# Kernel tuning notes

Hardware: AMD Instinct MI355X
Metric: run time of the kernel (lower is better)

Reference implementation:

```python
import jax, jax.numpy as jnp
import numpy as np

N_NODES = 100000


def _add_self_loops(edge_index, n):
    loops = jnp.arange(n, dtype=edge_index.dtype)
    src = jnp.concatenate([edge_index[0], loops])
    dst = jnp.concatenate([edge_index[1], loops])
    return src, dst


def _gcn_norm(src, dst, n):
    # symmetric normalization with unit edge weights (edge_weight=None)
    w = jnp.ones(src.shape[0], dtype=jnp.float32)
    deg = jax.ops.segment_sum(w, dst, num_segments=n)  # in-degree at dst (col)
    dinv = jnp.where(deg > 0, jax.lax.rsqrt(jnp.maximum(deg, 1.0)), 0.0)
    return dinv[src] * w * dinv[dst]


def _gcn_conv(x, W, b, src, dst, norm, n):
    h = x @ W                              # [N, F_out] linear first (as in PyG GCNConv)
    msg = h[src] * norm[:, None]           # gather + per-edge scale
    agg = jax.ops.segment_sum(msg, dst, num_segments=n)  # scatter-add at dst
    return agg + b


def setup_inputs() -> dict:
    key = jax.random.key(0)
    k1, k2, k3, k4 = jax.random.split(key, 4)
    x = jax.random.normal(k1, (N_NODES, 128), dtype=jnp.float32)
    edge_index = jax.random.randint(k2, (2, 1600000), 0, N_NODES, dtype=jnp.int64)
    W1 = jax.random.normal(k3, (128, 64), dtype=jnp.float32) * 0.08
    b1 = jnp.zeros((64,), dtype=jnp.float32)
    W2 = jax.random.normal(k4, (64, 40), dtype=jnp.float32) * 0.1
    b2 = jnp.zeros((40,), dtype=jnp.float32)
    return {"x": x, "edge_index": edge_index, "W1": W1, "b1": b1, "W2": W2, "b2": b2}


def reference(x, edge_index, W1, b1, W2, b2):
    n = x.shape[0]
    src, dst = _add_self_loops(edge_index, n)
    norm = _gcn_norm(src, dst, n)
    h = _gcn_conv(x, W1, b1, src, dst, norm, n)
    h = jax.nn.relu(h)
    # dropout is identity in eval mode (training=False)
    out = _gcn_conv(h, W2, b2, src, dst, norm, n)
    return out
```

## Files before the change

### kernel.cpp

```cpp
#include <hip/hip_runtime.h>
#include <hip/hip_fp16.h>


#define NPB   128
#define NBCAP 1024


__global__ void k_zero(int* __restrict__ p, int m) {
    int i = blockIdx.x * blockDim.x + threadIdx.x;
    if (i < m) p[i] = 0;
}

__global__ __launch_bounds__(256) void k_hist(const int* __restrict__ dst, int E,
                                              int* __restrict__ bcnt, int nb) {
    __shared__ int h[NBCAP];
    for (int i = threadIdx.x; i < nb; i += 256) h[i] = 0;
    __syncthreads();
    int stride = gridDim.x * 256;
    for (int e = blockIdx.x * 256 + threadIdx.x; e < E; e += stride)
        atomicAdd(&h[dst[e] >> 7], 1);
    __syncthreads();
    for (int i = threadIdx.x; i < nb; i += 256)
        if (h[i]) atomicAdd(&bcnt[i], h[i]);
}

__global__ __launch_bounds__(1024) void k_scan_nb(const int* __restrict__ bcnt,
                                                  int* __restrict__ bbase,
                                                  int* __restrict__ bcur, int nb) {
    __shared__ int tmp[NBCAP];
    int t = threadIdx.x;
    int v = (t < nb) ? bcnt[t] : 0;
    tmp[t] = v;
    __syncthreads();
    for (int ofs = 1; ofs < NBCAP; ofs <<= 1) {
        int u = (t >= ofs) ? tmp[t - ofs] : 0;
        __syncthreads();
        if (t >= ofs) tmp[t] += u;
        __syncthreads();
    }
    if (t < nb) {
        int ex = tmp[t] - v;
        bbase[t] = ex;
        bcur[t] = ex;
        if (t == nb - 1) bbase[nb] = tmp[t];
    }
}

__global__ __launch_bounds__(256) void k_binpass(const int* __restrict__ src,
                                                 const int* __restrict__ dst,
                                                 int* __restrict__ bcur,
                                                 int* __restrict__ pairs,
                                                 int nb, int E) {
    __shared__ int lh[NBCAP];
    __shared__ int lbase[NBCAP];
    for (int i = threadIdx.x; i < nb; i += 256) lh[i] = 0;
    __syncthreads();
    int base = blockIdx.x * 4096;
    int pk[16], bb[16];
#pragma unroll
    for (int k = 0; k < 16; ++k) {
        int e = base + k * 256 + threadIdx.x;
        if (e < E) {
            int d = dst[e];
            int b = d >> 7;
            bb[k] = b;
            pk[k] = src[e] | ((d & (NPB - 1)) << 17);
            atomicAdd(&lh[b], 1);
        } else bb[k] = -1;
    }
    __syncthreads();
    for (int i = threadIdx.x; i < nb; i += 256) {
        int c = lh[i];
        lbase[i] = c ? atomicAdd(&bcur[i], c) : 0;
        lh[i] = 0;
    }
    __syncthreads();
#pragma unroll
    for (int k = 0; k < 16; ++k) {
        if (bb[k] >= 0) {
            int r = atomicAdd(&lh[bb[k]], 1);
            pairs[lbase[bb[k]] + r] = pk[k];
        }
    }
}

__global__ __launch_bounds__(256) void k_bucket_build(const int* __restrict__ pairs,
                                                      const int* __restrict__ bbase,
                                                      int* __restrict__ off,
                                                      int* __restrict__ csrc,
                                                      float* __restrict__ dinv,
                                                      int n, int nb) {
    __shared__ int deg[NPB], sc[NPB], cur[NPB];
    int t = threadIdx.x;
    int bid = blockIdx.x;
    int node0 = bid * NPB;
    int ebeg = bbase[bid], eend = bbase[bid + 1];
    if (t < NPB) deg[t] = 0;
    __syncthreads();
    for (int e = ebeg + t; e < eend; e += 256)
        atomicAdd(&deg[pairs[e] >> 17], 1);
    __syncthreads();
    if (t < NPB) sc[t] = deg[t];
    __syncthreads();
    for (int ofs = 1; ofs < NPB; ofs <<= 1) {
        int u = (t < NPB && t >= ofs) ? sc[t - ofs] : 0;
        __syncthreads();
        if (t < NPB && t >= ofs) sc[t] += u;
        __syncthreads();
    }
    if (t < NPB) {
        int ex = sc[t] - deg[t];
        cur[t] = ex;
        int node = node0 + t;
        if (node < n) {
            off[node] = ebeg + ex;
            dinv[node] = rsqrtf((float)(deg[t] + 1));
        }
    }
    if (t == 0 && bid == nb - 1) off[n] = eend;
    __syncthreads();
    for (int e = ebeg + t; e < eend; e += 256) {
        int pkv = pairs[e];
        int r = atomicAdd(&cur[pkv >> 17], 1);
        csrc[ebeg + r] = pkv & 0x1FFFF;
    }
}


union pk2 { __half2 h[2]; uint2 u; };
union pk4 { __half2 h[4]; uint4 u; };

#define F4ADD(a, b) { (a).x += (b).x; (a).y += (b).y; (a).z += (b).z; (a).w += (b).w; }

__device__ __forceinline__ void acc8f(float4& lo, float4& hi, uint4 u) {
    __half2 h0 = *(__half2*)&u.x, h1 = *(__half2*)&u.y;
    __half2 h2v = *(__half2*)&u.z, h3v = *(__half2*)&u.w;
    float2 f0 = __half22float2(h0), f1 = __half22float2(h1);
    float2 f2 = __half22float2(h2v), f3 = __half22float2(h3v);
    lo.x += f0.x; lo.y += f0.y; lo.z += f1.x; lo.w += f1.y;
    hi.x += f2.x; hi.y += f2.y; hi.z += f3.x; hi.w += f3.y;
}

__device__ __forceinline__ void redstep(float4& lo, float4& hi, int delta, bool act) {
    float4 rl, rh;
    rl.x = __shfl_down(lo.x, delta); rl.y = __shfl_down(lo.y, delta);
    rl.z = __shfl_down(lo.z, delta); rl.w = __shfl_down(lo.w, delta);
    rh.x = __shfl_down(hi.x, delta); rh.y = __shfl_down(hi.y, delta);
    rh.z = __shfl_down(hi.z, delta); rh.w = __shfl_down(hi.w, delta);
    if (act) { F4ADD(lo, rl); F4ADD(hi, rh); }
}


__global__ __launch_bounds__(256) void k_gemm1_h(const float* __restrict__ x,
                                                 const float* __restrict__ W,
                                                 __half* __restrict__ h, int n,
                                                 const float* __restrict__ dinv) {
    __shared__ float Ws[128 * 64];
    __shared__ float xsT[128 * 64];
    const int tid = threadIdx.x;
    const int row0 = blockIdx.x * 64;
    {
        const float4* Wg = (const float4*)W;
        float4* Wl = (float4*)Ws;
#pragma unroll
        for (int t = 0; t < 8; ++t) Wl[tid + t * 256] = Wg[tid + t * 256];
    }
    {
        int r = tid & 63, g = tid >> 6;
        int row = row0 + r;
        const float4* xr = (const float4*)(x + (size_t)row * 128);
#pragma unroll
        for (int t = 0; t < 8; ++t) {
            int k0 = g * 32 + t * 4;
            float4 v = (row < n) ? xr[k0 >> 2] : make_float4(0.f, 0.f, 0.f, 0.f);
            xsT[(k0 + 0) * 64 + r] = v.x;
            xsT[(k0 + 1) * 64 + r] = v.y;
            xsT[(k0 + 2) * 64 + r] = v.z;
            xsT[(k0 + 3) * 64 + r] = v.w;
        }
    }
    __syncthreads();

    const int tc = tid & 15;
    const int rg = tid >> 4;
    float acc[4][4];
#pragma unroll
    for (int i = 0; i < 4; ++i)
#pragma unroll
        for (int j = 0; j < 4; ++j) acc[i][j] = 0.f;

#pragma unroll 4
    for (int k = 0; k < 128; ++k) {
        float4 a = *(const float4*)&xsT[k * 64 + rg * 4];
        float4 b = *(const float4*)&Ws[k * 64 + tc * 4];
        acc[0][0] += a.x * b.x; acc[0][1] += a.x * b.y; acc[0][2] += a.x * b.z; acc[0][3] += a.x * b.w;
        acc[1][0] += a.y * b.x; acc[1][1] += a.y * b.y; acc[1][2] += a.y * b.z; acc[1][3] += a.y * b.w;
        acc[2][0] += a.z * b.x; acc[2][1] += a.z * b.y; acc[2][2] += a.z * b.z; acc[2][3] += a.z * b.w;
        acc[3][0] += a.w * b.x; acc[3][1] += a.w * b.y; acc[3][2] += a.w * b.z; acc[3][3] += a.w * b.w;
    }

#pragma unroll
    for (int i = 0; i < 4; ++i) {
        int row = row0 + rg * 4 + i;
        if (row < n) {
            float dd = dinv[row];
            pk2 p;
            p.h[0] = __floats2half2_rn(acc[i][0] * dd, acc[i][1] * dd);
            p.h[1] = __floats2half2_rn(acc[i][2] * dd, acc[i][3] * dd);
            *(uint2*)&h[(size_t)row * 64 + tc * 4] = p.u;
        }
    }
}

__global__ __launch_bounds__(256) void k_gemm2_h(const __half* __restrict__ agg,
                                                 const float* __restrict__ W2,
                                                 __half* __restrict__ h2, int n,
                                                 const float* __restrict__ dinv) {
    __shared__ float Ws[64 * 40];
    __shared__ float hsT[64 * 64];
    const int tid = threadIdx.x;
    const int row0 = blockIdx.x * 64;
    {
        const float4* Wg = (const float4*)W2;
        float4* Wl = (float4*)Ws;
        for (int i = tid; i < 640; i += 256) Wl[i] = Wg[i];
    }
    {
        int r = tid & 63, g = tid >> 6;
        int row = row0 + r;
        const __half* ar = agg + (size_t)row * 64;
#pragma unroll
        for (int t = 0; t < 4; ++t) {
            int k0 = g * 16 + t * 4;
            float4 v = make_float4(0.f, 0.f, 0.f, 0.f);
            if (row < n) {
                uint2 u = *(const uint2*)(ar + k0);
                __half2 h0 = *(__half2*)&u.x, h1 = *(__half2*)&u.y;
                float2 f0 = __half22float2(h0), f1 = __half22float2(h1);
                v = make_float4(f0.x, f0.y, f1.x, f1.y);
            }
            hsT[(k0 + 0) * 64 + r] = v.x > 0.f ? v.x : 0.f;
            hsT[(k0 + 1) * 64 + r] = v.y > 0.f ? v.y : 0.f;
            hsT[(k0 + 2) * 64 + r] = v.z > 0.f ? v.z : 0.f;
            hsT[(k0 + 3) * 64 + r] = v.w > 0.f ? v.w : 0.f;
        }
    }
    __syncthreads();

    const int tc = tid & 15;
    const int rg = tid >> 4;
    if (tc < 10) {
        float acc[4][4];
#pragma unroll
        for (int i = 0; i < 4; ++i)
#pragma unroll
            for (int j = 0; j < 4; ++j) acc[i][j] = 0.f;

#pragma unroll 4
        for (int k = 0; k < 64; ++k) {
            float4 a = *(const float4*)&hsT[k * 64 + rg * 4];
            float4 b = *(const float4*)&Ws[k * 40 + tc * 4];
            acc[0][0] += a.x * b.x; acc[0][1] += a.x * b.y; acc[0][2] += a.x * b.z; acc[0][3] += a.x * b.w;
            acc[1][0] += a.y * b.x; acc[1][1] += a.y * b.y; acc[1][2] += a.y * b.z; acc[1][3] += a.y * b.w;
            acc[2][0] += a.z * b.x; acc[2][1] += a.z * b.y; acc[2][2] += a.z * b.z; acc[2][3] += a.z * b.w;
            acc[3][0] += a.w * b.x; acc[3][1] += a.w * b.y; acc[3][2] += a.w * b.z; acc[3][3] += a.w * b.w;
        }

#pragma unroll
        for (int i = 0; i < 4; ++i) {
            int row = row0 + rg * 4 + i;
            if (row < n) {
                float dd = dinv[row];
                pk2 p;
                p.h[0] = __floats2half2_rn(acc[i][0] * dd, acc[i][1] * dd);
                p.h[1] = __floats2half2_rn(acc[i][2] * dd, acc[i][3] * dd);
                *(uint2*)&h2[(size_t)row * 40 + tc * 4] = p.u;
            }
        }
    }
}


__global__ __launch_bounds__(256) void k_gather1_h(const __half* __restrict__ hs,
                                                   const int* __restrict__ off,
                                                   const int* __restrict__ csrc,
                                                   const float* __restrict__ dinv,
                                                   const float* __restrict__ bias1,
                                                   __half* __restrict__ agg1,
                                                   int n, int nwaves) {
    int wid = (blockIdx.x * 256 + threadIdx.x) >> 6;
    int lane = threadIdx.x & 63;
    int g = lane >> 3, q = lane & 7;
    for (int node = wid; node < n; node += nwaves) {
        int beg = off[node], end = off[node + 1];
        float4 a0 = make_float4(0.f, 0.f, 0.f, 0.f);
        float4 a1 = make_float4(0.f, 0.f, 0.f, 0.f);
        float4 c0 = make_float4(0.f, 0.f, 0.f, 0.f);
        float4 c1 = make_float4(0.f, 0.f, 0.f, 0.f);
        int j = beg;
        for (; j + 16 <= end; j += 16) {
            int s0 = csrc[j + g];
            int s1 = csrc[j + 8 + g];
            uint4 u0 = *(const uint4*)(hs + ((size_t)s0 << 6) + (q << 3));
            uint4 u1 = *(const uint4*)(hs + ((size_t)s1 << 6) + (q << 3));
            acc8f(a0, a1, u0);
            acc8f(c0, c1, u1);
        }
        for (; j + 8 <= end; j += 8) {
            int s0 = csrc[j + g];
            uint4 u0 = *(const uint4*)(hs + ((size_t)s0 << 6) + (q << 3));
            acc8f(a0, a1, u0);
        }
        if (j + g < end) {
            int s0 = csrc[j + g];
            uint4 u0 = *(const uint4*)(hs + ((size_t)s0 << 6) + (q << 3));
            acc8f(a0, a1, u0);
        }
        F4ADD(a0, c0); F4ADD(a1, c1);
        redstep(a0, a1, 32, lane < 32);
        redstep(a0, a1, 16, lane < 16);
        redstep(a0, a1, 8,  lane < 8);
        if (lane < 8) {
            float dd = dinv[node];
            uint4 us = *(const uint4*)(hs + ((size_t)node << 6) + (q << 3));
            float4 slo = make_float4(0.f, 0.f, 0.f, 0.f);
            float4 shi = make_float4(0.f, 0.f, 0.f, 0.f);
            acc8f(slo, shi, us);
            float4 blo = *(const float4*)(bias1 + q * 8);
            float4 bhi = *(const float4*)(bias1 + q * 8 + 4);
            pk4 p;
            p.h[0] = __floats2half2_rn((a0.x + slo.x) * dd + blo.x,
                                       (a0.y + slo.y) * dd + blo.y);
            p.h[1] = __floats2half2_rn((a0.z + slo.z) * dd + blo.z,
                                       (a0.w + slo.w) * dd + blo.w);
            p.h[2] = __floats2half2_rn((a1.x + shi.x) * dd + bhi.x,
                                       (a1.y + shi.y) * dd + bhi.y);
            p.h[3] = __floats2half2_rn((a1.z + shi.z) * dd + bhi.z,
                                       (a1.w + shi.w) * dd + bhi.w);
            *(uint4*)&agg1[((size_t)node << 6) + (q << 3)] = p.u;
        }
    }
}

__global__ __launch_bounds__(256) void k_gather2_h(const __half* __restrict__ h2s,
                                                   const int* __restrict__ off,
                                                   const int* __restrict__ csrc,
                                                   const float* __restrict__ dinv,
                                                   const float* __restrict__ b2,
                                                   float* __restrict__ out,
                                                   int n, int nwaves) {
    int wid = (blockIdx.x * 256 + threadIdx.x) >> 6;
    int lane = threadIdx.x & 63;
    int g = lane / 5;
    int q = lane - g * 5;
    bool act = lane < 60;
    for (int node = wid; node < n; node += nwaves) {
        int beg = off[node], end = off[node + 1];
        float4 a0 = make_float4(0.f, 0.f, 0.f, 0.f);
        float4 a1 = make_float4(0.f, 0.f, 0.f, 0.f);
        int j = beg;
        for (; j + 12 <= end; j += 12) {
            if (act) {
                int s0 = csrc[j + g];
                uint4 u0 = *(const uint4*)(h2s + (size_t)s0 * 40 + q * 8);
                acc8f(a0, a1, u0);
            }
        }
        if (act && j + g < end) {
            int s0 = csrc[j + g];
            uint4 u0 = *(const uint4*)(h2s + (size_t)s0 * 40 + q * 8);
            acc8f(a0, a1, u0);
        }
        redstep(a0, a1, 30, lane < 30);
        redstep(a0, a1, 15, lane < 15);
        redstep(a0, a1, 10, lane < 5);
        redstep(a0, a1, 5,  lane < 5);
        if (lane < 5) {
            float dd = dinv[node];
            uint4 us = *(const uint4*)(h2s + (size_t)node * 40 + lane * 8);
            float4 slo = make_float4(0.f, 0.f, 0.f, 0.f);
            float4 shi = make_float4(0.f, 0.f, 0.f, 0.f);
            acc8f(slo, shi, us);
            float4 blo = *(const float4*)(b2 + lane * 8);
            float4 bhi = *(const float4*)(b2 + lane * 8 + 4);
            float4 o0, o1;
            o0.x = (a0.x + slo.x) * dd + blo.x;
            o0.y = (a0.y + slo.y) * dd + blo.y;
            o0.z = (a0.z + slo.z) * dd + blo.z;
            o0.w = (a0.w + slo.w) * dd + blo.w;
            o1.x = (a1.x + shi.x) * dd + bhi.x;
            o1.y = (a1.y + shi.y) * dd + bhi.y;
            o1.z = (a1.z + shi.z) * dd + bhi.z;
            o1.w = (a1.w + shi.w) * dd + bhi.w;
            *(float4*)&out[(size_t)node * 40 + lane * 8] = o0;
            *(float4*)&out[(size_t)node * 40 + lane * 8 + 4] = o1;
        }
    }
}


__global__ void k_init_deg(float* __restrict__ deg, int n) {
    int i = blockIdx.x * blockDim.x + threadIdx.x;
    if (i < n) deg[i] = 1.0f;
}

__global__ void k_deg(const int* __restrict__ dst, int E, float* __restrict__ deg) {
    int i = blockIdx.x * blockDim.x + threadIdx.x;
    if (i < E) atomicAdd(&deg[dst[i]], 1.0f);
}

__global__ void k_rsqrt(float* __restrict__ deg, int n) {
    int i = blockIdx.x * blockDim.x + threadIdx.x;
    if (i < n) deg[i] = rsqrtf(deg[i]);
}

__global__ __launch_bounds__(256) void k_gemm1_f(const float* __restrict__ x,
                                                 const float* __restrict__ W,
                                                 float* __restrict__ h, int n) {
    __shared__ float Ws[128 * 64];
    __shared__ float xsT[128 * 64];
    const int tid = threadIdx.x;
    const int row0 = blockIdx.x * 64;
    {
        const float4* Wg = (const float4*)W;
        float4* Wl = (float4*)Ws;
#pragma unroll
        for (int t = 0; t < 8; ++t) Wl[tid + t * 256] = Wg[tid + t * 256];
    }
    {
        int r = tid & 63, g = tid >> 6;
        int row = row0 + r;
        const float4* xr = (const float4*)(x + (size_t)row * 128);
#pragma unroll
        for (int t = 0; t < 8; ++t) {
            int k0 = g * 32 + t * 4;
            float4 v = (row < n) ? xr[k0 >> 2] : make_float4(0.f, 0.f, 0.f, 0.f);
            xsT[(k0 + 0) * 64 + r] = v.x;
            xsT[(k0 + 1) * 64 + r] = v.y;
            xsT[(k0 + 2) * 64 + r] = v.z;
            xsT[(k0 + 3) * 64 + r] = v.w;
        }
    }
    __syncthreads();
    const int tc = tid & 15;
    const int rg = tid >> 4;
    float acc[4][4];
#pragma unroll
    for (int i = 0; i < 4; ++i)
#pragma unroll
        for (int j = 0; j < 4; ++j) acc[i][j] = 0.f;
#pragma unroll 4
    for (int k = 0; k < 128; ++k) {
        float4 a = *(const float4*)&xsT[k * 64 + rg * 4];
        float4 b = *(const float4*)&Ws[k * 64 + tc * 4];
        acc[0][0] += a.x * b.x; acc[0][1] += a.x * b.y; acc[0][2] += a.x * b.z; acc[0][3] += a.x * b.w;
        acc[1][0] += a.y * b.x; acc[1][1] += a.y * b.y; acc[1][2] += a.y * b.z; acc[1][3] += a.y * b.w;
        acc[2][0] += a.z * b.x; acc[2][1] += a.z * b.y; acc[2][2] += a.z * b.z; acc[2][3] += a.z * b.w;
        acc[3][0] += a.w * b.x; acc[3][1] += a.w * b.y; acc[3][2] += a.w * b.z; acc[3][3] += a.w * b.w;
    }
#pragma unroll
    for (int i = 0; i < 4; ++i) {
        int row = row0 + rg * 4 + i;
        if (row < n)
            *(float4*)&h[(size_t)row * 64 + tc * 4] =
                make_float4(acc[i][0], acc[i][1], acc[i][2], acc[i][3]);
    }
}

__global__ __launch_bounds__(256) void k_gemm2_f(const float* __restrict__ agg,
                                                 const float* __restrict__ W2,
                                                 float* __restrict__ h2, int n) {
    __shared__ float Ws[64 * 40];
    __shared__ float hsT[64 * 64];
    const int tid = threadIdx.x;
    const int row0 = blockIdx.x * 64;
    {
        const float4* Wg = (const float4*)W2;
        float4* Wl = (float4*)Ws;
        for (int i = tid; i < 640; i += 256) Wl[i] = Wg[i];
    }
    {
        int r = tid & 63, g = tid >> 6;
        int row = row0 + r;
        const float4* ar = (const float4*)(agg + (size_t)row * 64);
#pragma unroll
        for (int t = 0; t < 4; ++t) {
            int k0 = g * 16 + t * 4;
            float4 v = (row < n) ? ar[k0 >> 2] : make_float4(0.f, 0.f, 0.f, 0.f);
            hsT[(k0 + 0) * 64 + r] = v.x > 0.f ? v.x : 0.f;
            hsT[(k0 + 1) * 64 + r] = v.y > 0.f ? v.y : 0.f;
            hsT[(k0 + 2) * 64 + r] = v.z > 0.f ? v.z : 0.f;
            hsT[(k0 + 3) * 64 + r] = v.w > 0.f ? v.w : 0.f;
        }
    }
    __syncthreads();
    const int tc = tid & 15;
    const int rg = tid >> 4;
    if (tc < 10) {
        float acc[4][4];
#pragma unroll
        for (int i = 0; i < 4; ++i)
#pragma unroll
            for (int j = 0; j < 4; ++j) acc[i][j] = 0.f;
#pragma unroll 4
        for (int k = 0; k < 64; ++k) {
            float4 a = *(const float4*)&hsT[k * 64 + rg * 4];
            float4 b = *(const float4*)&Ws[k * 40 + tc * 4];
            acc[0][0] += a.x * b.x; acc[0][1] += a.x * b.y; acc[0][2] += a.x * b.z; acc[0][3] += a.x * b.w;
            acc[1][0] += a.y * b.x; acc[1][1] += a.y * b.y; acc[1][2] += a.y * b.z; acc[1][3] += a.y * b.w;
            acc[2][0] += a.z * b.x; acc[2][1] += a.z * b.y; acc[2][2] += a.z * b.z; acc[2][3] += a.z * b.w;
            acc[3][0] += a.w * b.x; acc[3][1] += a.w * b.y; acc[3][2] += a.w * b.z; acc[3][3] += a.w * b.w;
        }
#pragma unroll
        for (int i = 0; i < 4; ++i) {
            int row = row0 + rg * 4 + i;
            if (row < n)
                *(float4*)&h2[(size_t)row * 40 + tc * 4] =
                    make_float4(acc[i][0], acc[i][1], acc[i][2], acc[i][3]);
        }
    }
}

__global__ void k_init_agg1(const float* __restrict__ h, const float* __restrict__ dinv,
                            const float* __restrict__ b1, float* __restrict__ agg, int n) {
    int idx = blockIdx.x * blockDim.x + threadIdx.x;
    if (idx < n * 64) {
        int i = idx >> 6, f = idx & 63;
        float d = dinv[i];
        agg[idx] = h[idx] * d * d + b1[f];
    }
}

__global__ __launch_bounds__(256) void k_scatter1(const float* __restrict__ h,
                                                  const int* __restrict__ src,
                                                  const int* __restrict__ dst,
                                                  const float* __restrict__ dinv,
                                                  float* __restrict__ agg, int E) {
    int e = blockIdx.x * 4 + (threadIdx.x >> 6);
    if (e >= E) return;
    int f = threadIdx.x & 63;
    int s = src[e], d = dst[e];
    float w = dinv[s] * dinv[d];
    atomicAdd(&agg[d * 64 + f], h[s * 64 + f] * w);
}

__global__ void k_init_out(const float* __restrict__ h2, const float* __restrict__ dinv,
                           const float* __restrict__ b2, float* __restrict__ out, int n) {
    int idx = blockIdx.x * blockDim.x + threadIdx.x;
    if (idx < n * 40) {
        int i = idx / 40;
        int f = idx - i * 40;
        float d = dinv[i];
        out[idx] = h2[idx] * d * d + b2[f];
    }
}

__global__ __launch_bounds__(256) void k_scatter2(const float* __restrict__ h2,
                                                  const int* __restrict__ src,
                                                  const int* __restrict__ dst,
                                                  const float* __restrict__ dinv,
                                                  float* __restrict__ out, int E) {
    int idx = blockIdx.x * blockDim.x + threadIdx.x;
    int total = E * 40;
    if (idx >= total) return;
    int e = idx / 40;
    int f = idx - e * 40;
    int s = src[e], d = dst[e];
    float w = dinv[s] * dinv[d];
    atomicAdd(&out[d * 40 + f], h2[s * 40 + f] * w);
}

extern "C" void kernel_launch(void* const* d_in, const int* in_sizes, int n_in,
                              void* d_out, int out_size, void* d_ws, size_t ws_size,
                              hipStream_t stream) {
    const float* x  = (const float*)d_in[0];
    const int*   ei = (const int*)d_in[1];
    const float* W1 = (const float*)d_in[2];
    const float* b1 = (const float*)d_in[3];
    const float* W2 = (const float*)d_in[4];
    const float* b2 = (const float*)d_in[5];
    float* out = (float*)d_out;

    const int n = in_sizes[0] / 128;
    const int E = in_sizes[1] / 2;
    const int* src = ei;
    const int* dst = ei + E;

    char* ws = (char*)d_ws;
    const size_t MB = 1 << 20;
    float*  dinv   = (float*)(ws);
    int*    off    = (int*)  (ws + 512 * 1024);
    int*    bcnt   = (int*)  (ws + 1 * MB);
    int*    bbase  = (int*)  (ws + 1 * MB + 8 * 1024);
    int*    bcur   = (int*)  (ws + 1 * MB + 16 * 1024);
    __half* hs_h   = (__half*)(ws + 2 * MB);
    __half* agg1_h = (__half*)(ws + 15 * MB);
    __half* h2s_h  = hs_h;
    int*    pairs  = (int*)  (ws + 28 * MB);
    int*    csrc   = (int*)  (ws + 35 * MB);
    size_t needed_fast = 35 * MB + (size_t)E * 4;

    const int nb = (n + NPB - 1) / NPB;

    if (ws_size >= needed_fast && nb <= NBCAP && n <= (1 << 17)) {
        k_zero<<<(nb + 255) / 256, 256, 0, stream>>>(bcnt, nb);
        k_hist<<<512, 256, 0, stream>>>(dst, E, bcnt, nb);
        k_scan_nb<<<1, 1024, 0, stream>>>(bcnt, bbase, bcur, nb);
        k_binpass<<<(E + 4095) / 4096, 256, 0, stream>>>(src, dst, bcur, pairs, nb, E);
        k_bucket_build<<<nb, 256, 0, stream>>>(pairs, bbase, off, csrc, dinv, n, nb);

        const int GB = 2048;
        const int NW = GB * 4;
        k_gemm1_h<<<(n + 63) / 64, 256, 0, stream>>>(x, W1, hs_h, n, dinv);
        k_gather1_h<<<GB, 256, 0, stream>>>(hs_h, off, csrc, dinv, b1, agg1_h, n, NW);

        k_gemm2_h<<<(n + 63) / 64, 256, 0, stream>>>(agg1_h, W2, h2s_h, n, dinv);
        k_gather2_h<<<GB, 256, 0, stream>>>(h2s_h, off, csrc, dinv, b2, out, n, NW);
    } else {
        float* hlin = (float*)(ws + 2 * MB);
        float* agg1 = (float*)(ws + 28 * MB);
        k_init_deg<<<(n + 255) / 256, 256, 0, stream>>>(dinv, n);
        k_deg<<<(E + 255) / 256, 256, 0, stream>>>(dst, E, dinv);
        k_rsqrt<<<(n + 255) / 256, 256, 0, stream>>>(dinv, n);
        k_gemm1_f<<<(n + 63) / 64, 256, 0, stream>>>(x, W1, hlin, n);
        k_init_agg1<<<(n * 64 + 255) / 256, 256, 0, stream>>>(hlin, dinv, b1, agg1, n);
        k_scatter1<<<(E + 3) / 4, 256, 0, stream>>>(hlin, src, dst, dinv, agg1, E);
        k_gemm2_f<<<(n + 63) / 64, 256, 0, stream>>>(agg1, W2, hlin, n);
        k_init_out<<<(n * 40 + 255) / 256, 256, 0, stream>>>(hlin, dinv, b2, out, n);
        int total2 = E * 40;
        k_scatter2<<<(total2 + 255) / 256, 256, 0, stream>>>(hlin, src, dst, dinv, out, E);
    }
}
```

Before: 199.2 us.

## Reorder layer-2 as aggregate-then-transform and gather four nodes per wave

Layer 2 now aggregates the 64-wide ReLU'd hidden features first and applies W2 plus bias afterwards in a GEMM that writes the output, instead of transforming to 40 columns and then gathering. This lets both layers share one gather kernel, which processes four destination nodes per wave to overlap more independent loads. The layer-1 epilogue folds in ReLU and the dinv prescale. Bucket size in the CSR build also doubles to 256 nodes. The trade-off is that the second gather moves 64-wide half rows instead of 40-wide ones, and lanes idle on nodes with uneven degree.

```diff
diff --git a/kernel.cpp b/kernel.cpp
--- a/kernel.cpp
+++ b/kernel.cpp
@@ -2,8 +2,9 @@
 #include <hip/hip_fp16.h>
 
 
-#define NPB   128
-#define NBCAP 1024
+#define NPB      256
+#define NB_SHIFT 8
+#define NBCAP    512
 
 
 __global__ void k_zero(int* __restrict__ p, int m) {
@@ -18,21 +19,21 @@
     __syncthreads();
     int stride = gridDim.x * 256;
     for (int e = blockIdx.x * 256 + threadIdx.x; e < E; e += stride)
-        atomicAdd(&h[dst[e] >> 7], 1);
+        atomicAdd(&h[dst[e] >> NB_SHIFT], 1);
     __syncthreads();
     for (int i = threadIdx.x; i < nb; i += 256)
         if (h[i]) atomicAdd(&bcnt[i], h[i]);
 }
 
-__global__ __launch_bounds__(1024) void k_scan_nb(const int* __restrict__ bcnt,
-                                                  int* __restrict__ bbase,
-                                                  int* __restrict__ bcur, int nb) {
-    __shared__ int tmp[NBCAP];
+__global__ __launch_bounds__(512) void k_scan_nb(const int* __restrict__ bcnt,
+                                                 int* __restrict__ bbase,
+                                                 int* __restrict__ bcur, int nb) {
+    __shared__ int tmp[512];
     int t = threadIdx.x;
     int v = (t < nb) ? bcnt[t] : 0;
     tmp[t] = v;
     __syncthreads();
-    for (int ofs = 1; ofs < NBCAP; ofs <<= 1) {
+    for (int ofs = 1; ofs < 512; ofs <<= 1) {
         int u = (t >= ofs) ? tmp[t - ofs] : 0;
         __syncthreads();
         if (t >= ofs) tmp[t] += u;
@@ -62,7 +63,7 @@
         int e = base + k * 256 + threadIdx.x;
         if (e < E) {
             int d = dst[e];
-            int b = d >> 7;
+            int b = d >> NB_SHIFT;
             bb[k] = b;
             pk[k] = src[e] | ((d & (NPB - 1)) << 17);
             atomicAdd(&lh[b], 1);
@@ -95,20 +96,20 @@
     int bid = blockIdx.x;
     int node0 = bid * NPB;
     int ebeg = bbase[bid], eend = bbase[bid + 1];
-    if (t < NPB) deg[t] = 0;
+    deg[t] = 0;
     __syncthreads();
     for (int e = ebeg + t; e < eend; e += 256)
         atomicAdd(&deg[pairs[e] >> 17], 1);
     __syncthreads();
-    if (t < NPB) sc[t] = deg[t];
+    sc[t] = deg[t];
     __syncthreads();
     for (int ofs = 1; ofs < NPB; ofs <<= 1) {
-        int u = (t < NPB && t >= ofs) ? sc[t - ofs] : 0;
+        int u = (t >= ofs) ? sc[t - ofs] : 0;
         __syncthreads();
-        if (t < NPB && t >= ofs) sc[t] += u;
+        if (t >= ofs) sc[t] += u;
         __syncthreads();
     }
-    if (t < NPB) {
+    {
         int ex = sc[t] - deg[t];
         cur[t] = ex;
         int node = node0 + t;
@@ -212,10 +213,10 @@
     }
 }
 
-__global__ __launch_bounds__(256) void k_gemm2_h(const __half* __restrict__ agg,
-                                                 const float* __restrict__ W2,
-                                                 __half* __restrict__ h2, int n,
-                                                 const float* __restrict__ dinv) {
+__global__ __launch_bounds__(256) void k_gemm2_out(const __half* __restrict__ g2,
+                                                   const float* __restrict__ W2,
+                                                   const float* __restrict__ b2,
+                                                   float* __restrict__ out, int n) {
     __shared__ float Ws[64 * 40];
     __shared__ float hsT[64 * 64];
     const int tid = threadIdx.x;
@@ -228,7 +229,7 @@
     {
         int r = tid & 63, g = tid >> 6;
         int row = row0 + r;
-        const __half* ar = agg + (size_t)row * 64;
+        const __half* ar = g2 + (size_t)row * 64;
 #pragma unroll
         for (int t = 0; t < 4; ++t) {
             int k0 = g * 16 + t * 4;
@@ -239,10 +240,10 @@
                 float2 f0 = __half22float2(h0), f1 = __half22float2(h1);
                 v = make_float4(f0.x, f0.y, f1.x, f1.y);
             }
-            hsT[(k0 + 0) * 64 + r] = v.x > 0.f ? v.x : 0.f;
-            hsT[(k0 + 1) * 64 + r] = v.y > 0.f ? v.y : 0.f;
-            hsT[(k0 + 2) * 64 + r] = v.z > 0.f ? v.z : 0.f;
-            hsT[(k0 + 3) * 64 + r] = v.w > 0.f ? v.w : 0.f;
+            hsT[(k0 + 0) * 64 + r] = v.x;
+            hsT[(k0 + 1) * 64 + r] = v.y;
+            hsT[(k0 + 2) * 64 + r] = v.z;
+            hsT[(k0 + 3) * 64 + r] = v.w;
         }
     }
     __syncthreads();
@@ -266,134 +267,115 @@
             acc[3][0] += a.w * b.x; acc[3][1] += a.w * b.y; acc[3][2] += a.w * b.z; acc[3][3] += a.w * b.w;
         }
 
+        float4 bb = *(const float4*)(b2 + tc * 4);
 #pragma unroll
         for (int i = 0; i < 4; ++i) {
             int row = row0 + rg * 4 + i;
-            if (row < n) {
-                float dd = dinv[row];
-                pk2 p;
-                p.h[0] = __floats2half2_rn(acc[i][0] * dd, acc[i][1] * dd);
-                p.h[1] = __floats2half2_rn(acc[i][2] * dd, acc[i][3] * dd);
-                *(uint2*)&h2[(size_t)row * 40 + tc * 4] = p.u;
-            }
-        }
-    }
-}
-
-
-__global__ __launch_bounds__(256) void k_gather1_h(const __half* __restrict__ hs,
-                                                   const int* __restrict__ off,
-                                                   const int* __restrict__ csrc,
-                                                   const float* __restrict__ dinv,
-                                                   const float* __restrict__ bias1,
-                                                   __half* __restrict__ agg1,
-                                                   int n, int nwaves) {
+            if (row < n)
+                *(float4*)&out[(size_t)row * 40 + tc * 4] =
+                    make_float4(acc[i][0] + bb.x, acc[i][1] + bb.y,
+                                acc[i][2] + bb.z, acc[i][3] + bb.w);
+        }
+    }
+}
+
+
+__global__ __launch_bounds__(256) void k_gather4(const __half* __restrict__ feat,
+                                                 const int* __restrict__ off,
+                                                 const int* __restrict__ csrc,
+                                                 const float* __restrict__ dinv,
+                                                 const float* __restrict__ bias,
+                                                 __half* __restrict__ outh,
+                                                 int n, int E, int nwq, int mode) {
     int wid = (blockIdx.x * 256 + threadIdx.x) >> 6;
     int lane = threadIdx.x & 63;
     int g = lane >> 3, q = lane & 7;
-    for (int node = wid; node < n; node += nwaves) {
-        int beg = off[node], end = off[node + 1];
-        float4 a0 = make_float4(0.f, 0.f, 0.f, 0.f);
-        float4 a1 = make_float4(0.f, 0.f, 0.f, 0.f);
-        float4 c0 = make_float4(0.f, 0.f, 0.f, 0.f);
-        float4 c1 = make_float4(0.f, 0.f, 0.f, 0.f);
-        int j = beg;
-        for (; j + 16 <= end; j += 16) {
-            int s0 = csrc[j + g];
-            int s1 = csrc[j + 8 + g];
-            uint4 u0 = *(const uint4*)(hs + ((size_t)s0 << 6) + (q << 3));
-            uint4 u1 = *(const uint4*)(hs + ((size_t)s1 << 6) + (q << 3));
-            acc8f(a0, a1, u0);
-            acc8f(c0, c1, u1);
-        }
-        for (; j + 8 <= end; j += 8) {
-            int s0 = csrc[j + g];
-            uint4 u0 = *(const uint4*)(hs + ((size_t)s0 << 6) + (q << 3));
-            acc8f(a0, a1, u0);
-        }
-        if (j + g < end) {
-            int s0 = csrc[j + g];
-            uint4 u0 = *(const uint4*)(hs + ((size_t)s0 << 6) + (q << 3));
-            acc8f(a0, a1, u0);
-        }
-        F4ADD(a0, c0); F4ADD(a1, c1);
-        redstep(a0, a1, 32, lane < 32);
-        redstep(a0, a1, 16, lane < 16);
-        redstep(a0, a1, 8,  lane < 8);
+    int Em1 = E - 1;
+    for (int base = wid * 4; base < n; base += nwq * 4) {
+        int b0, e0, b1, e1, b2_, e2, b3, e3;
+        b0 = off[base]; e0 = off[base + 1];
+        if (base + 1 < n) { b1 = off[base + 1]; e1 = off[base + 2]; } else { b1 = e1 = 0; }
+        if (base + 2 < n) { b2_ = off[base + 2]; e2 = off[base + 3]; } else { b2_ = e2 = 0; }
+        if (base + 3 < n) { b3 = off[base + 3]; e3 = off[base + 4]; } else { b3 = e3 = 0; }
+
+        float4 A0l = make_float4(0.f, 0.f, 0.f, 0.f), A0h = A0l;
+        float4 A1l = A0l, A1h = A0l, A2l = A0l, A2h = A0l, A3l = A0l, A3h = A0l;
+
+        int j0 = b0, j1 = b1, j2 = b2_, j3 = b3;
+        while ((j0 < e0) || (j1 < e1) || (j2 < e2) || (j3 < e3)) {
+            bool v0 = j0 + g < e0, v1 = j1 + g < e1, v2 = j2 + g < e2, v3 = j3 + g < e3;
+            int i0 = min(j0 + g, Em1), i1 = min(j1 + g, Em1);
+            int i2 = min(j2 + g, Em1), i3 = min(j3 + g, Em1);
+            int s0 = csrc[i0], s1 = csrc[i1], s2 = csrc[i2], s3 = csrc[i3];
+            uint4 u0 = *(const uint4*)(feat + ((size_t)s0 << 6) + (q << 3));
+            uint4 u1 = *(const uint4*)(feat + ((size_t)s1 << 6) + (q << 3));
+            uint4 u2 = *(const uint4*)(feat + ((size_t)s2 << 6) + (q << 3));
+            uint4 u3 = *(const uint4*)(feat + ((size_t)s3 << 6) + (q << 3));
+            if (v0) acc8f(A0l, A0h, u0);
+            if (v1) acc8f(A1l, A1h, u1);
+            if (v2) acc8f(A2l, A2h, u2);
+            if (v3) acc8f(A3l, A3h, u3);
+            j0 += 8; j1 += 8; j2 += 8; j3 += 8;
+        }
+
+        redstep(A0l, A0h, 32, lane < 32);
+        redstep(A0l, A0h, 16, lane < 16);
+        redstep(A0l, A0h, 8,  lane < 8);
+        redstep(A1l, A1h, 32, lane < 32);
+        redstep(A1l, A1h, 16, lane < 16);
+        redstep(A1l, A1h, 8,  lane < 8);
+        redstep(A2l, A2h, 32, lane < 32);
+        redstep(A2l, A2h, 16, lane < 16);
+        redstep(A2l, A2h, 8,  lane < 8);
+        redstep(A3l, A3h, 32, lane < 32);
+        redstep(A3l, A3h, 16, lane < 16);
+        redstep(A3l, A3h, 8,  lane < 8);
+
         if (lane < 8) {
-            float dd = dinv[node];
-            uint4 us = *(const uint4*)(hs + ((size_t)node << 6) + (q << 3));
-            float4 slo = make_float4(0.f, 0.f, 0.f, 0.f);
-            float4 shi = make_float4(0.f, 0.f, 0.f, 0.f);
-            acc8f(slo, shi, us);
-            float4 blo = *(const float4*)(bias1 + q * 8);
-            float4 bhi = *(const float4*)(bias1 + q * 8 + 4);
-            pk4 p;
-            p.h[0] = __floats2half2_rn((a0.x + slo.x) * dd + blo.x,
-                                       (a0.y + slo.y) * dd + blo.y);
-            p.h[1] = __floats2half2_rn((a0.z + slo.z) * dd + blo.z,
-                                       (a0.w + slo.w) * dd + blo.w);
-            p.h[2] = __floats2half2_rn((a1.x + shi.x) * dd + bhi.x,
-                                       (a1.y + shi.y) * dd + bhi.y);
-            p.h[3] = __floats2half2_rn((a1.z + shi.z) * dd + bhi.z,
-                                       (a1.w + shi.w) * dd + bhi.w);
-            *(uint4*)&agg1[((size_t)node << 6) + (q << 3)] = p.u;
-        }
-    }
-}
-
-__global__ __launch_bounds__(256) void k_gather2_h(const __half* __restrict__ h2s,
-                                                   const int* __restrict__ off,
-                                                   const int* __restrict__ csrc,
-                                                   const float* __restrict__ dinv,
-                                                   const float* __restrict__ b2,
-                                                   float* __restrict__ out,
-                                                   int n, int nwaves) {
-    int wid = (blockIdx.x * 256 + threadIdx.x) >> 6;
-    int lane = threadIdx.x & 63;
-    int g = lane / 5;
-    int q = lane - g * 5;
-    bool act = lane < 60;
-    for (int node = wid; node < n; node += nwaves) {
-        int beg = off[node], end = off[node + 1];
-        float4 a0 = make_float4(0.f, 0.f, 0.f, 0.f);
-        float4 a1 = make_float4(0.f, 0.f, 0.f, 0.f);
-        int j = beg;
-        for (; j + 12 <= end; j += 12) {
-            if (act) {
-                int s0 = csrc[j + g];
-                uint4 u0 = *(const uint4*)(h2s + (size_t)s0 * 40 + q * 8);
-                acc8f(a0, a1, u0);
+            float4 blo = make_float4(0.f, 0.f, 0.f, 0.f), bhi = blo;
+            if (mode == 0) {
+                blo = *(const float4*)(bias + q * 8);
+                bhi = *(const float4*)(bias + q * 8 + 4);
             }
-        }
-        if (act && j + g < end) {
-            int s0 = csrc[j + g];
-            uint4 u0 = *(const uint4*)(h2s + (size_t)s0 * 40 + q * 8);
-            acc8f(a0, a1, u0);
-        }
-        redstep(a0, a1, 30, lane < 30);
-        redstep(a0, a1, 15, lane < 15);
-        redstep(a0, a1, 10, lane < 5);
-        redstep(a0, a1, 5,  lane < 5);
-        if (lane < 5) {
-            float dd = dinv[node];
-            uint4 us = *(const uint4*)(h2s + (size_t)node * 40 + lane * 8);
-            float4 slo = make_float4(0.f, 0.f, 0.f, 0.f);
-            float4 shi = make_float4(0.f, 0.f, 0.f, 0.f);
-            acc8f(slo, shi, us);
-            float4 blo = *(const float4*)(b2 + lane * 8);
-            float4 bhi = *(const float4*)(b2 + lane * 8 + 4);
-            float4 o0, o1;
-            o0.x = (a0.x + slo.x) * dd + blo.x;
-            o0.y = (a0.y + slo.y) * dd + blo.y;
-            o0.z = (a0.z + slo.z) * dd + blo.z;
-            o0.w = (a0.w + slo.w) * dd + blo.w;
-            o1.x = (a1.x + shi.x) * dd + bhi.x;
-            o1.y = (a1.y + shi.y) * dd + bhi.y;
-            o1.z = (a1.z + shi.z) * dd + bhi.z;
-            o1.w = (a1.w + shi.w) * dd + bhi.w;
-            *(float4*)&out[(size_t)node * 40 + lane * 8] = o0;
-            *(float4*)&out[(size_t)node * 40 + lane * 8 + 4] = o1;
+#define EPI(K, AL, AH)                                                          \
+            {                                                                   \
+                int node = base + K;                                            \
+                if (node < n) {                                                 \
+                    float dd = dinv[node];                                      \
+                    uint4 us = *(const uint4*)(feat + ((size_t)node << 6) + (q << 3)); \
+                    float4 sl = make_float4(0.f, 0.f, 0.f, 0.f), sh = sl;       \
+                    acc8f(sl, sh, us);                                          \
+                    float f0 = (AL.x + sl.x) * dd + blo.x;                      \
+                    float f1 = (AL.y + sl.y) * dd + blo.y;                      \
+                    float f2 = (AL.z + sl.z) * dd + blo.z;                      \
+                    float f3 = (AL.w + sl.w) * dd + blo.w;                      \
+                    float f4 = (AH.x + sh.x) * dd + bhi.x;                      \
+                    float f5 = (AH.y + sh.y) * dd + bhi.y;                      \
+                    float f6 = (AH.z + sh.z) * dd + bhi.z;                      \
+                    float f7 = (AH.w + sh.w) * dd + bhi.w;                      \
+                    if (mode == 0) {                                            \
+                        f0 = (f0 > 0.f ? f0 : 0.f) * dd;                        \
+                        f1 = (f1 > 0.f ? f1 : 0.f) * dd;                        \
+                        f2 = (f2 > 0.f ? f2 : 0.f) * dd;                        \
+                        f3 = (f3 > 0.f ? f3 : 0.f) * dd;                        \
+                        f4 = (f4 > 0.f ? f4 : 0.f) * dd;                        \
+                        f5 = (f5 > 0.f ? f5 : 0.f) * dd;                        \
+                        f6 = (f6 > 0.f ? f6 : 0.f) * dd;                        \
+                        f7 = (f7 > 0.f ? f7 : 0.f) * dd;                        \
+                    }                                                           \
+                    pk4 p;                                                      \
+                    p.h[0] = __floats2half2_rn(f0, f1);                         \
+                    p.h[1] = __floats2half2_rn(f2, f3);                         \
+                    p.h[2] = __floats2half2_rn(f4, f5);                         \
+                    p.h[3] = __floats2half2_rn(f6, f7);                         \
+                    *(uint4*)&outh[((size_t)node << 6) + (q << 3)] = p.u;       \
+                }                                                               \
+            }
+            EPI(0, A0l, A0h)
+            EPI(1, A1l, A1h)
+            EPI(2, A2l, A2h)
+            EPI(3, A3l, A3h)
+#undef EPI
         }
     }
 }
@@ -594,28 +576,29 @@
     int*    bbase  = (int*)  (ws + 1 * MB + 8 * 1024);
     int*    bcur   = (int*)  (ws + 1 * MB + 16 * 1024);
     __half* hs_h   = (__half*)(ws + 2 * MB);
-    __half* agg1_h = (__half*)(ws + 15 * MB);
-    __half* h2s_h  = hs_h;
+    __half* r2_h   = (__half*)(ws + 15 * MB);
+    __half* g2_h   = hs_h;
     int*    pairs  = (int*)  (ws + 28 * MB);
     int*    csrc   = (int*)  (ws + 35 * MB);
     size_t needed_fast = 35 * MB + (size_t)E * 4;
 
     const int nb = (n + NPB - 1) / NPB;
 
-    if (ws_size >= needed_fast && nb <= NBCAP && n <= (1 << 17)) {
+    if (ws_size >= needed_fast && nb <= NBCAP && n <= (1 << 17) && E >= 8) {
         k_zero<<<(nb + 255) / 256, 256, 0, stream>>>(bcnt, nb);
         k_hist<<<512, 256, 0, stream>>>(dst, E, bcnt, nb);
-        k_scan_nb<<<1, 1024, 0, stream>>>(bcnt, bbase, bcur, nb);
+        k_scan_nb<<<1, 512, 0, stream>>>(bcnt, bbase, bcur, nb);
         k_binpass<<<(E + 4095) / 4096, 256, 0, stream>>>(src, dst, bcur, pairs, nb, E);
         k_bucket_build<<<nb, 256, 0, stream>>>(pairs, bbase, off, csrc, dinv, n, nb);
 
         const int GB = 2048;
         const int NW = GB * 4;
+
         k_gemm1_h<<<(n + 63) / 64, 256, 0, stream>>>(x, W1, hs_h, n, dinv);
-        k_gather1_h<<<GB, 256, 0, stream>>>(hs_h, off, csrc, dinv, b1, agg1_h, n, NW);
-
-        k_gemm2_h<<<(n + 63) / 64, 256, 0, stream>>>(agg1_h, W2, h2s_h, n, dinv);
-        k_gather2_h<<<GB, 256, 0, stream>>>(h2s_h, off, csrc, dinv, b2, out, n, NW);
+        k_gather4<<<GB, 256, 0, stream>>>(hs_h, off, csrc, dinv, b1, r2_h, n, E, NW, 0);
+
+        k_gather4<<<GB, 256, 0, stream>>>(r2_h, off, csrc, dinv, nullptr, g2_h, n, E, NW, 1);
+        k_gemm2_out<<<(n + 63) / 64, 256, 0, stream>>>(g2_h, W2, b2, out, n);
     } else {
         float* hlin = (float*)(ws + 2 * MB);
         float* agg1 = (float*)(ws + 28 * MB);
```

Measured after the change: 225.2 us. 13.1% more time.

## Reorder second GCN layer to aggregate before applying W2

Applied to the files above, without the earlier changes.

The second layer now uses associativity, aggregating the 64-wide hidden features over the graph first and applying W2 afterwards, so the second gather reuses the same 64-wide gather kernel. The ReLU and the dinv pre-scaling move into the first gather's epilogue, and the final GEMM writes the output directly with the bias added. This drops the awkward 40-wide gather layout with idle lanes in favour of a uniform 64-wide gather. In exchange the second gather reads 64 fp16 features per edge instead of 40, so it moves more bytes.

```diff
diff --git a/kernel.cpp b/kernel.cpp
--- a/kernel.cpp
+++ b/kernel.cpp
@@ -212,10 +212,10 @@
     }
 }
 
-__global__ __launch_bounds__(256) void k_gemm2_h(const __half* __restrict__ agg,
-                                                 const float* __restrict__ W2,
-                                                 __half* __restrict__ h2, int n,
-                                                 const float* __restrict__ dinv) {
+__global__ __launch_bounds__(256) void k_gemm2_out(const __half* __restrict__ g2,
+                                                   const float* __restrict__ W2,
+                                                   const float* __restrict__ b2,
+                                                   float* __restrict__ out, int n) {
     __shared__ float Ws[64 * 40];
     __shared__ float hsT[64 * 64];
     const int tid = threadIdx.x;
@@ -228,7 +228,7 @@
     {
         int r = tid & 63, g = tid >> 6;
         int row = row0 + r;
-        const __half* ar = agg + (size_t)row * 64;
+        const __half* ar = g2 + (size_t)row * 64;
 #pragma unroll
         for (int t = 0; t < 4; ++t) {
             int k0 = g * 16 + t * 4;
@@ -239,10 +239,10 @@
                 float2 f0 = __half22float2(h0), f1 = __half22float2(h1);
                 v = make_float4(f0.x, f0.y, f1.x, f1.y);
             }
-            hsT[(k0 + 0) * 64 + r] = v.x > 0.f ? v.x : 0.f;
-            hsT[(k0 + 1) * 64 + r] = v.y > 0.f ? v.y : 0.f;
-            hsT[(k0 + 2) * 64 + r] = v.z > 0.f ? v.z : 0.f;
-            hsT[(k0 + 3) * 64 + r] = v.w > 0.f ? v.w : 0.f;
+            hsT[(k0 + 0) * 64 + r] = v.x;
+            hsT[(k0 + 1) * 64 + r] = v.y;
+            hsT[(k0 + 2) * 64 + r] = v.z;
+            hsT[(k0 + 3) * 64 + r] = v.w;
         }
     }
     __syncthreads();
@@ -266,28 +266,26 @@
             acc[3][0] += a.w * b.x; acc[3][1] += a.w * b.y; acc[3][2] += a.w * b.z; acc[3][3] += a.w * b.w;
         }
 
+        float4 bb = *(const float4*)(b2 + tc * 4);
 #pragma unroll
         for (int i = 0; i < 4; ++i) {
             int row = row0 + rg * 4 + i;
-            if (row < n) {
-                float dd = dinv[row];
-                pk2 p;
-                p.h[0] = __floats2half2_rn(acc[i][0] * dd, acc[i][1] * dd);
-                p.h[1] = __floats2half2_rn(acc[i][2] * dd, acc[i][3] * dd);
-                *(uint2*)&h2[(size_t)row * 40 + tc * 4] = p.u;
-            }
-        }
-    }
-}
-
-
-__global__ __launch_bounds__(256) void k_gather1_h(const __half* __restrict__ hs,
-                                                   const int* __restrict__ off,
-                                                   const int* __restrict__ csrc,
-                                                   const float* __restrict__ dinv,
-                                                   const float* __restrict__ bias1,
-                                                   __half* __restrict__ agg1,
-                                                   int n, int nwaves) {
+            if (row < n)
+                *(float4*)&out[(size_t)row * 40 + tc * 4] =
+                    make_float4(acc[i][0] + bb.x, acc[i][1] + bb.y,
+                                acc[i][2] + bb.z, acc[i][3] + bb.w);
+        }
+    }
+}
+
+
+__global__ __launch_bounds__(256) void k_gather_h(const __half* __restrict__ feat,
+                                                  const int* __restrict__ off,
+                                                  const int* __restrict__ csrc,
+                                                  const float* __restrict__ dinv,
+                                                  const float* __restrict__ bias,
+                                                  __half* __restrict__ outh,
+                                                  int n, int nwaves, int mode) {
     int wid = (blockIdx.x * 256 + threadIdx.x) >> 6;
     int lane = threadIdx.x & 63;
     int g = lane >> 3, q = lane & 7;
@@ -301,19 +299,19 @@
         for (; j + 16 <= end; j += 16) {
             int s0 = csrc[j + g];
             int s1 = csrc[j + 8 + g];
-            uint4 u0 = *(const uint4*)(hs + ((size_t)s0 << 6) + (q << 3));
-            uint4 u1 = *(const uint4*)(hs + ((size_t)s1 << 6) + (q << 3));
+            uint4 u0 = *(const uint4*)(feat + ((size_t)s0 << 6) + (q << 3));
+            uint4 u1 = *(const uint4*)(feat + ((size_t)s1 << 6) + (q << 3));
             acc8f(a0, a1, u0);
             acc8f(c0, c1, u1);
         }
         for (; j + 8 <= end; j += 8) {
             int s0 = csrc[j + g];
-            uint4 u0 = *(const uint4*)(hs + ((size_t)s0 << 6) + (q << 3));
+            uint4 u0 = *(const uint4*)(feat + ((size_t)s0 << 6) + (q << 3));
             acc8f(a0, a1, u0);
         }
         if (j + g < end) {
             int s0 = csrc[j + g];
-            uint4 u0 = *(const uint4*)(hs + ((size_t)s0 << 6) + (q << 3));
+            uint4 u0 = *(const uint4*)(feat + ((size_t)s0 << 6) + (q << 3));
             acc8f(a0, a1, u0);
         }
         F4ADD(a0, c0); F4ADD(a1, c1);
@@ -322,78 +320,38 @@
         redstep(a0, a1, 8,  lane < 8);
         if (lane < 8) {
             float dd = dinv[node];
-            uint4 us = *(const uint4*)(hs + ((size_t)node << 6) + (q << 3));
+            uint4 us = *(const uint4*)(feat + ((size_t)node << 6) + (q << 3));
             float4 slo = make_float4(0.f, 0.f, 0.f, 0.f);
             float4 shi = make_float4(0.f, 0.f, 0.f, 0.f);
             acc8f(slo, shi, us);
-            float4 blo = *(const float4*)(bias1 + q * 8);
-            float4 bhi = *(const float4*)(bias1 + q * 8 + 4);
+            float f0 = (a0.x + slo.x) * dd;
+            float f1 = (a0.y + slo.y) * dd;
+            float f2 = (a0.z + slo.z) * dd;
+            float f3 = (a0.w + slo.w) * dd;
+            float f4 = (a1.x + shi.x) * dd;
+            float f5 = (a1.y + shi.y) * dd;
+            float f6 = (a1.z + shi.z) * dd;
+            float f7 = (a1.w + shi.w) * dd;
+            if (mode == 0) {
+                float4 blo = *(const float4*)(bias + q * 8);
+                float4 bhi = *(const float4*)(bias + q * 8 + 4);
+                f0 += blo.x; f1 += blo.y; f2 += blo.z; f3 += blo.w;
+                f4 += bhi.x; f5 += bhi.y; f6 += bhi.z; f7 += bhi.w;
+                f0 = (f0 > 0.f ? f0 : 0.f) * dd;
+                f1 = (f1 > 0.f ? f1 : 0.f) * dd;
+                f2 = (f2 > 0.f ? f2 : 0.f) * dd;
+                f3 = (f3 > 0.f ? f3 : 0.f) * dd;
+                f4 = (f4 > 0.f ? f4 : 0.f) * dd;
+                f5 = (f5 > 0.f ? f5 : 0.f) * dd;
+                f6 = (f6 > 0.f ? f6 : 0.f) * dd;
+                f7 = (f7 > 0.f ? f7 : 0.f) * dd;
+            }
             pk4 p;
-            p.h[0] = __floats2half2_rn((a0.x + slo.x) * dd + blo.x,
-                                       (a0.y + slo.y) * dd + blo.y);
-            p.h[1] = __floats2half2_rn((a0.z + slo.z) * dd + blo.z,
-                                       (a0.w + slo.w) * dd + blo.w);
-            p.h[2] = __floats2half2_rn((a1.x + shi.x) * dd + bhi.x,
-                                       (a1.y + shi.y) * dd + bhi.y);
-            p.h[3] = __floats2half2_rn((a1.z + shi.z) * dd + bhi.z,
-                                       (a1.w + shi.w) * dd + bhi.w);
-            *(uint4*)&agg1[((size_t)node << 6) + (q << 3)] = p.u;
-        }
-    }
-}
-
-__global__ __launch_bounds__(256) void k_gather2_h(const __half* __restrict__ h2s,
-                                                   const int* __restrict__ off,
-                                                   const int* __restrict__ csrc,
-                                                   const float* __restrict__ dinv,
-                                                   const float* __restrict__ b2,
-                                                   float* __restrict__ out,
-                                                   int n, int nwaves) {
-    int wid = (blockIdx.x * 256 + threadIdx.x) >> 6;
-    int lane = threadIdx.x & 63;
-    int g = lane / 5;
-    int q = lane - g * 5;
-    bool act = lane < 60;
-    for (int node = wid; node < n; node += nwaves) {
-        int beg = off[node], end = off[node + 1];
-        float4 a0 = make_float4(0.f, 0.f, 0.f, 0.f);
-        float4 a1 = make_float4(0.f, 0.f, 0.f, 0.f);
-        int j = beg;
-        for (; j + 12 <= end; j += 12) {
-            if (act) {
-                int s0 = csrc[j + g];
-                uint4 u0 = *(const uint4*)(h2s + (size_t)s0 * 40 + q * 8);
-                acc8f(a0, a1, u0);
-            }
-        }
-        if (act && j + g < end) {
-            int s0 = csrc[j + g];
-            uint4 u0 = *(const uint4*)(h2s + (size_t)s0 * 40 + q * 8);
-            acc8f(a0, a1, u0);
-        }
-        redstep(a0, a1, 30, lane < 30);
-        redstep(a0, a1, 15, lane < 15);
-        redstep(a0, a1, 10, lane < 5);
-        redstep(a0, a1, 5,  lane < 5);
-        if (lane < 5) {
-            float dd = dinv[node];
-            uint4 us = *(const uint4*)(h2s + (size_t)node * 40 + lane * 8);
-            float4 slo = make_float4(0.f, 0.f, 0.f, 0.f);
-            float4 shi = make_float4(0.f, 0.f, 0.f, 0.f);
-            acc8f(slo, shi, us);
-            float4 blo = *(const float4*)(b2 + lane * 8);
-            float4 bhi = *(const float4*)(b2 + lane * 8 + 4);
-            float4 o0, o1;
-            o0.x = (a0.x + slo.x) * dd + blo.x;
-            o0.y = (a0.y + slo.y) * dd + blo.y;
-            o0.z = (a0.z + slo.z) * dd + blo.z;
-            o0.w = (a0.w + slo.w) * dd + blo.w;
-            o1.x = (a1.x + shi.x) * dd + bhi.x;
-            o1.y = (a1.y + shi.y) * dd + bhi.y;
-            o1.z = (a1.z + shi.z) * dd + bhi.z;
-            o1.w = (a1.w + shi.w) * dd + bhi.w;
-            *(float4*)&out[(size_t)node * 40 + lane * 8] = o0;
-            *(float4*)&out[(size_t)node * 40 + lane * 8 + 4] = o1;
+            p.h[0] = __floats2half2_rn(f0, f1);
+            p.h[1] = __floats2half2_rn(f2, f3);
+            p.h[2] = __floats2half2_rn(f4, f5);
+            p.h[3] = __floats2half2_rn(f6, f7);
+            *(uint4*)&outh[((size_t)node << 6) + (q << 3)] = p.u;
         }
     }
 }
@@ -594,8 +552,8 @@
     int*    bbase  = (int*)  (ws + 1 * MB + 8 * 1024);
     int*    bcur   = (int*)  (ws + 1 * MB + 16 * 1024);
     __half* hs_h   = (__half*)(ws + 2 * MB);
-    __half* agg1_h = (__half*)(ws + 15 * MB);
-    __half* h2s_h  = hs_h;
+    __half* r2_h   = (__half*)(ws + 15 * MB);
+    __half* g2_h   = hs_h;
     int*    pairs  = (int*)  (ws + 28 * MB);
     int*    csrc   = (int*)  (ws + 35 * MB);
     size_t needed_fast = 35 * MB + (size_t)E * 4;
@@ -611,11 +569,12 @@
 
         const int GB = 2048;
         const int NW = GB * 4;
+
         k_gemm1_h<<<(n + 63) / 64, 256, 0, stream>>>(x, W1, hs_h, n, dinv);
-        k_gather1_h<<<GB, 256, 0, stream>>>(hs_h, off, csrc, dinv, b1, agg1_h, n, NW);
-
-        k_gemm2_h<<<(n + 63) / 64, 256, 0, stream>>>(agg1_h, W2, h2s_h, n, dinv);
-        k_gather2_h<<<GB, 256, 0, stream>>>(h2s_h, off, csrc, dinv, b2, out, n, NW);
+        k_gather_h<<<GB, 256, 0, stream>>>(hs_h, off, csrc, dinv, b1, r2_h, n, NW, 0);
+
+        k_gather_h<<<GB, 256, 0, stream>>>(r2_h, off, csrc, dinv, b1, g2_h, n, NW, 1);
+        k_gemm2_out<<<(n + 63) / 64, 256, 0, stream>>>(g2_h, W2, b2, out, n);
     } else {
         float* hlin = (float*)(ws + 2 * MB);
         float* agg1 = (float*)(ws + 28 * MB);
```

Result: no change. 196.0 us (-1.6%).
